# Kernel tuning notes

Hardware: AMD Instinct MI355X
Metric: run time of the kernel (lower is better)

## Reference

```python
import jax, jax.numpy as jnp
import numpy as np

BATCH, N_FEAT, N_CH = 16384, 16, 1
EXP_ORDER, OUT_DIM = 3, 256


def expansion_indices(n, exp_order):
    """Replicates the original nested-loop index bookkeeping statically.

    Returns a list of (J, P) per expansion pass: the new block of monomials is
    x[:, J, :] * epd[:, P, :]. All indices in a pass reference terms produced in
    earlier passes, so one concat per pass is exactly equivalent to the original.
    """
    Id = np.arange(n)
    M = n
    steps = []
    for _ in range(exp_order):
        Js, Ps = [], []
        for j in range(n):
            rng = np.arange(Id[j], Id[n - 1] + 1)
            Js.append(np.full(rng.shape, j))
            Ps.append(rng)
            Id[j] = M
            M += rng.size
        steps.append((np.concatenate(Js), np.concatenate(Ps)))
    return steps, M

STEPS, M_TOTAL = expansion_indices(N_FEAT, EXP_ORDER)  # M_TOTAL == 4844


def taylor_expand(x):
    # x: [B, n, Q] -> epd: [B, M_TOTAL, Q] (all monomials of degree 1..EXP_ORDER+1)
    epd = x
    for J, P in STEPS:
        new = x[:, J, :] * epd[:, P, :]
        epd = jnp.concatenate([epd, new], axis=1)
    return epd


def setup_inputs() -> dict:
    key = jax.random.key(0)
    k1, k2, k3 = jax.random.split(key, 3)
    inputs = jax.random.normal(k1, (BATCH, N_FEAT, N_CH), dtype=jnp.float32)
    # 'dl' weight init: uniform(-1/sqrt(shape[0]), 1/sqrt(shape[0]))
    w_scale = 1.0 / np.sqrt(OUT_DIM)
    W = jax.random.uniform(k2, (OUT_DIM, M_TOTAL), minval=-w_scale, maxval=w_scale, dtype=jnp.float32)
    # 'uniform' bias init: uniform(-0.2, 0.2), shape [out, 1]
    b = jax.random.uniform(k3, (OUT_DIM, 1), minval=-0.2, maxval=0.2, dtype=jnp.float32)
    return {"inputs": inputs, "W": W, "b": b}


def reference(inputs, W, b):
    # cp_type='tanh': first cp block applies tanh, second block is identity for tanh
    x = jnp.tanh(inputs)
    epd = taylor_expand(x)                         # [B, M_TOTAL, Q]
    out = jnp.einsum('rm,bmq->brq', W, epd) + b    # [B, OUT_DIM, Q]
    return jax.nn.relu(out)                        # act_type='relu'
```

## Files before the change

kernel.cpp:

```cpp
#include <hip/hip_runtime.h>

#define BATCH   16384
#define NF      16
#define OUTD    256
#define NNEW    4828
#define MTOT    4844
#define KPAD    4864
#define KPAD2   (KPAD/2)
#define NCHUNK  76
#define TROW    155
#define ASTR    72

struct ExpTab { unsigned jp[NNEW]; int total; };

constexpr ExpTab make_tab() {
    ExpTab t{};
    int Id[NF] = {};
    for (int i = 0; i < NF; ++i) Id[i] = i;
    int M = NF, idx = 0;
    for (int pass = 0; pass < 3; ++pass) {
        const int hi = Id[NF - 1];
        for (int j = 0; j < NF; ++j) {
            const int lo = Id[j];
            for (int p = lo; p <= hi; ++p) t.jp[idx++] = ((unsigned)j << 16) | (unsigned)p;
            Id[j] = M;
            M += hi - lo + 1;
        }
    }
    t.total = M;
    return t;
}
constexpr ExpTab h_tab = make_tab();
static_assert(h_tab.total == MTOT, "M_TOTAL");

struct PkTab {
    alignas(16) unsigned e[KPAD];
    unsigned b2[136];
};

constexpr PkTab make_pk() {
    ExpTab t = make_tab();
    int d2[NF][NF] = {};
    {
        int m = NF;
        for (int j = 0; j < NF; ++j)
            for (int p = j; p < NF; ++p) d2[j][p] = m++;
    }
    PkTab pk{};
    for (int q = 0; q < 136; ++q) {
        unsigned jp = t.jp[q];
        pk.b2[q] = (jp >> 16) | ((jp & 0xffffu) << 16);
    }
    for (int m = 0; m < KPAD; ++m) {
        if (m >= MTOT) { pk.e[m] = 153u | (153u << 16); continue; }
        int f[4] = {}, n = 0, cur = m;
        while (cur >= NF) {
            unsigned jp = t.jp[cur - NF];
            f[n++] = (int)(jp >> 16);
            cur = (int)(jp & 0xffffu);
        }
        f[n++] = cur;
        for (int i = 0; i < n; ++i)
            for (int k = i + 1; k < n; ++k)
                if (f[k] < f[i]) { int tmp = f[i]; f[i] = f[k]; f[k] = tmp; }
        unsigned L, R;
        if      (n == 1) { L = (unsigned)f[0];         R = 152u; }
        else if (n == 2) { L = (unsigned)d2[f[0]][f[1]]; R = 152u; }
        else if (n == 3) { L = (unsigned)d2[f[0]][f[1]]; R = (unsigned)f[2]; }
        else             { L = (unsigned)d2[f[0]][f[1]]; R = (unsigned)d2[f[2]][f[3]]; }
        pk.e[m] = L | (R << 16);
    }
    return pk;
}
constexpr bool pk_ok() {
    PkTab p = make_pk();
    for (int m = 0; m < KPAD; ++m)
        if ((p.e[m] & 0xffffu) > 153u || (p.e[m] >> 16) > 153u) return false;
    return p.e[16] == (16u | (152u << 16));
}
static_assert(pk_ok(), "2-factor decomposition");

__device__ const PkTab g_pk = make_pk();

typedef __attribute__((ext_vector_type(8))) short    bf16x8;
typedef __attribute__((ext_vector_type(4))) float    f32x4;
typedef __attribute__((ext_vector_type(4))) unsigned uint4v;

__device__ inline unsigned bfpack2(float lo, float hi) {
    unsigned ul = __float_as_uint(lo), uh = __float_as_uint(hi);
    ul = (ul + 0x7fffu + ((ul >> 16) & 1u)) >> 16;
    uh = (uh + 0x7fffu + ((uh >> 16) & 1u)) & 0xffff0000u;
    return ul | uh;
}

__global__ __launch_bounds__(256) void wconv_kernel(
    const float* __restrict__ W, unsigned* __restrict__ Wb)
{
    const int r = blockIdx.x;
    for (int i = threadIdx.x; i < KPAD2; i += 256) {
        const int c0 = 2 * i, c1 = 2 * i + 1;
        const float f0 = (c0 < MTOT) ? W[(size_t)r * MTOT + c0] : 0.f;
        const float f1 = (c1 < MTOT) ? W[(size_t)r * MTOT + c1] : 0.f;
        Wb[(size_t)r * KPAD2 + i] = bfpack2(f0, f1);
    }
}

__global__ __launch_bounds__(512, 2) void fused_kernel(
    const float* __restrict__ x,
    const unsigned short* __restrict__ Wb,
    const float* __restrict__ bias,
    float* __restrict__ C)
{
    __shared__ float T[64 * TROW];
    __shared__ alignas(16) unsigned short As[2][64][ASTR];
    const int t   = threadIdx.x;
    const int l   = t & 63;
    const int wid = t >> 6;
    const size_t m0 = (size_t)blockIdx.x * 64;

    uint4v eA[4], eB[4];
    auto loadPk = [&](int c, uint4v (&e4)[4]) {
        const uint4v* pe = (const uint4v*)(g_pk.e + c * 64 + wid * 16);
#pragma unroll
        for (int i = 0; i < 4; ++i) e4[i] = pe[i];
    };
    if (wid < 4) loadPk(0, eA);

#pragma unroll
    for (int i = 0; i < 2; ++i) {
        const int v = t * 2 + i;
        const int r = v >> 4, fq = v & 15;
        T[r * TROW + fq] = tanhf(x[(m0 + r) * NF + fq]);
    }
    if (t < 64) { T[t * TROW + 152] = 1.0f; T[t * TROW + 153] = 0.0f; }
    __syncthreads();

    {
        const int r = t >> 3, s = t & 7, base = r * TROW;
#pragma unroll
        for (int i = 0; i < 17; ++i) {
            const int q = s + 8 * i;
            const unsigned e = g_pk.b2[q];
            T[base + NF + q] = T[base + (e & 0xffffu)] * T[base + (e >> 16)];
        }
    }
    __syncthreads();

    const int pbase = l * TROW;
    auto expand = [&](int slot, const uint4v (&e4)[4]) {
        float v[16];
#pragma unroll
        for (int i = 0; i < 16; ++i) {
            const unsigned e = e4[i >> 2][i & 3];
            v[i] = T[pbase + (e & 0xffffu)] * T[pbase + (e >> 16)];
        }
        uint4v o0, o1;
        o0[0] = bfpack2(v[0],  v[1]);  o0[1] = bfpack2(v[2],  v[3]);
        o0[2] = bfpack2(v[4],  v[5]);  o0[3] = bfpack2(v[6],  v[7]);
        o1[0] = bfpack2(v[8],  v[9]);  o1[1] = bfpack2(v[10], v[11]);
        o1[2] = bfpack2(v[12], v[13]); o1[3] = bfpack2(v[14], v[15]);
        *(uint4v*)&As[slot][l][wid * 16]     = o0;
        *(uint4v*)&As[slot][l][wid * 16 + 8] = o1;
    };

    const int w  = wid - 4;
    const int lr = l & 15, lk = l >> 4;
    const unsigned short* wbase = Wb + (size_t)(w * 64 + lr) * KPAD + lk * 8;
    bf16x8 bA[4][2], bB[4][2];
    auto prefB = [&](int c, bf16x8 (&bf)[4][2]) {
#pragma unroll
        for (int ni = 0; ni < 4; ++ni)
#pragma unroll
            for (int ks = 0; ks < 2; ++ks)
                bf[ni][ks] = *(const bf16x8*)(wbase + (size_t)ni * 16 * KPAD
                                              + (size_t)c * 64 + ks * 32);
    };
    f32x4 acc[4][4];
#pragma unroll
    for (int i = 0; i < 4; ++i)
#pragma unroll
        for (int j = 0; j < 4; ++j) acc[i][j] = (f32x4){0.f, 0.f, 0.f, 0.f};

    auto domfma = [&](int slot, bf16x8 (&bf)[4][2]) {
#pragma unroll
        for (int ks = 0; ks < 2; ++ks) {
            bf16x8 af[4];
#pragma unroll
            for (int mi = 0; mi < 4; ++mi)
                af[mi] = *(const bf16x8*)&As[slot][mi * 16 + lr][ks * 32 + lk * 8];
#pragma unroll
            for (int mi = 0; mi < 4; ++mi)
#pragma unroll
                for (int ni = 0; ni < 4; ++ni)
                    acc[mi][ni] = __builtin_amdgcn_mfma_f32_16x16x32_bf16(
                        af[mi], bf[ni][ks], acc[mi][ni], 0, 0, 0);
        }
    };

    if (wid < 4) { expand(0, eA); loadPk(1, eB); }
    else         { prefB(0, bA); }
    __syncthreads();

    for (int it = 0; it < NCHUNK / 2; ++it) {
        const int c = 2 * it;
        if (wid < 4) {
            if (c + 2 < NCHUNK) loadPk(c + 2, eA);
            expand(1, eB);
        } else {
            prefB(c + 1, bB);
            domfma(0, bA);
        }
        __syncthreads();
        if (wid < 4) {
            if (c + 3 < NCHUNK) loadPk(c + 3, eB);
            if (c + 2 < NCHUNK) expand(0, eA);
        } else {
            if (c + 2 < NCHUNK) prefB(c + 2, bA);
            domfma(1, bB);
        }
        __syncthreads();
    }

    if (wid >= 4) {
#pragma unroll
        for (int ni = 0; ni < 4; ++ni) {
            const int col = w * 64 + ni * 16 + lr;
            const float bv = bias[col];
#pragma unroll
            for (int mi = 0; mi < 4; ++mi) {
                const size_t r0 = m0 + mi * 16 + lk * 4;
#pragma unroll
                for (int j = 0; j < 4; ++j)
                    C[(r0 + j) * OUTD + col] = fmaxf(acc[mi][ni][j] + bv, 0.f);
            }
        }
    }
}

extern "C" void kernel_launch(void* const* d_in, const int* in_sizes, int n_in,
                              void* d_out, int out_size, void* d_ws, size_t ws_size,
                              hipStream_t stream)
{
    const float* x    = (const float*)d_in[0];
    const float* W    = (const float*)d_in[1];
    const float* bias = (const float*)d_in[2];
    float* out        = (float*)d_out;

    unsigned* Wb = (unsigned*)d_ws;
    wconv_kernel<<<OUTD, 256, 0, stream>>>(W, Wb);
    fused_kernel<<<BATCH / 64, 512, 0, stream>>>(
        x, (const unsigned short*)Wb, bias, out);
}
```

Baseline: 148.9 us.

## Halve batch tile to 32 rows with 2 producer and 4 MFMA waves

Each block now handles 32 batch rows instead of 64. It uses 384 threads: 2 waves expand monomials into LDS and 4 waves run MFMAs, with launch bounds changed to allow 3 blocks per CU. The A tile in LDS gets an XOR swizzle on 16-byte groups to cut bank conflicts, and the MFMA section is wrapped in s_setprio. The aim is more blocks (512 instead of 256) and better occupancy and latency hiding. The cost is that every W tile is reloaded from global/L2 for only 32 rows, doubling weight traffic per output.

```diff
diff --git a/kernel.cpp b/kernel.cpp
--- a/kernel.cpp
+++ b/kernel.cpp
@@ -8,6 +8,7 @@
 #define KPAD    4864
 #define KPAD2   (KPAD/2)
 #define NCHUNK  76
+#define BM      32
 #define TROW    155
 #define ASTR    72
 
@@ -64,7 +65,7 @@
             for (int k = i + 1; k < n; ++k)
                 if (f[k] < f[i]) { int tmp = f[i]; f[i] = f[k]; f[k] = tmp; }
         unsigned L, R;
-        if      (n == 1) { L = (unsigned)f[0];         R = 152u; }
+        if      (n == 1) { L = (unsigned)f[0];           R = 152u; }
         else if (n == 2) { L = (unsigned)d2[f[0]][f[1]]; R = 152u; }
         else if (n == 3) { L = (unsigned)d2[f[0]][f[1]]; R = (unsigned)f[2]; }
         else             { L = (unsigned)d2[f[0]][f[1]]; R = (unsigned)d2[f[2]][f[3]]; }
@@ -105,37 +106,54 @@
     }
 }
 
-__global__ __launch_bounds__(512, 2) void fused_kernel(
+__global__ __launch_bounds__(384, 3) void fused_kernel(
     const float* __restrict__ x,
     const unsigned short* __restrict__ Wb,
     const float* __restrict__ bias,
     float* __restrict__ C)
 {
-    __shared__ float T[64 * TROW];
-    __shared__ alignas(16) unsigned short As[2][64][ASTR];
+    __shared__ float T[BM * TROW];
+    __shared__ alignas(16) unsigned short As[2][BM * ASTR];
     const int t   = threadIdx.x;
     const int l   = t & 63;
     const int wid = t >> 6;
-    const size_t m0 = (size_t)blockIdx.x * 64;
-
+    const size_t m0 = (size_t)blockIdx.x * BM;
+
+    const int pr = l & 31;
+    const int ph = l >> 5;
     uint4v eA[4], eB[4];
     auto loadPk = [&](int c, uint4v (&e4)[4]) {
-        const uint4v* pe = (const uint4v*)(g_pk.e + c * 64 + wid * 16);
+        const uint4v* pe = (const uint4v*)(g_pk.e + c * 64 + wid * 32 + ph * 16);
 #pragma unroll
         for (int i = 0; i < 4; ++i) e4[i] = pe[i];
     };
-    if (wid < 4) loadPk(0, eA);
-
-#pragma unroll
-    for (int i = 0; i < 2; ++i) {
-        const int v = t * 2 + i;
-        const int r = v >> 4, fq = v & 15;
-        T[r * TROW + fq] = tanhf(x[(m0 + r) * NF + fq]);
-    }
-    if (t < 64) { T[t * TROW + 152] = 1.0f; T[t * TROW + 153] = 0.0f; }
+    if (wid < 2) loadPk(0, eA);
+
+    const int w  = wid - 2;
+    const int lr = l & 15, lk = l >> 4;
+    const unsigned short* wbase = Wb + (size_t)(w * 64 + lr) * KPAD + lk * 8;
+    bf16x8 bA[4][2], bB[4][2];
+    auto prefB = [&](int c, bf16x8 (&bf)[4][2]) {
+#pragma unroll
+        for (int ni = 0; ni < 4; ++ni)
+#pragma unroll
+            for (int ks = 0; ks < 2; ++ks)
+                bf[ni][ks] = *(const bf16x8*)(wbase + (size_t)ni * 16 * KPAD
+                                              + (size_t)c * 64 + ks * 32);
+    };
+    if (wid >= 2) prefB(0, bA);
+
+    if (t < 256) {
+#pragma unroll
+        for (int i = 0; i < 2; ++i) {
+            const int v = t * 2 + i;
+            const int r = v >> 4, fq = v & 15;
+            T[r * TROW + fq] = tanhf(x[(m0 + r) * NF + fq]);
+        }
+        if (t < BM) { T[t * TROW + 152] = 1.0f; T[t * TROW + 153] = 0.0f; }
+    }
     __syncthreads();
-
-    {
+    if (t < 256) {
         const int r = t >> 3, s = t & 7, base = r * TROW;
 #pragma unroll
         for (int i = 0; i < 17; ++i) {
@@ -146,7 +164,11 @@
     }
     __syncthreads();
 
-    const int pbase = l * TROW;
+    const int pbase = pr * TROW;
+    const int g0   = wid * 4 + ph * 2;
+    const int gswz = (pr >> 3) & 3;
+    const int wo0  = pr * ASTR + ((g0    ) ^ gswz) * 8;
+    const int wo1  = pr * ASTR + ((g0 + 1) ^ gswz) * 8;
     auto expand = [&](int slot, const uint4v (&e4)[4]) {
         float v[16];
 #pragma unroll
@@ -159,51 +181,44 @@
         o0[2] = bfpack2(v[4],  v[5]);  o0[3] = bfpack2(v[6],  v[7]);
         o1[0] = bfpack2(v[8],  v[9]);  o1[1] = bfpack2(v[10], v[11]);
         o1[2] = bfpack2(v[12], v[13]); o1[3] = bfpack2(v[14], v[15]);
-        *(uint4v*)&As[slot][l][wid * 16]     = o0;
-        *(uint4v*)&As[slot][l][wid * 16 + 8] = o1;
-    };
-
-    const int w  = wid - 4;
-    const int lr = l & 15, lk = l >> 4;
-    const unsigned short* wbase = Wb + (size_t)(w * 64 + lr) * KPAD + lk * 8;
-    bf16x8 bA[4][2], bB[4][2];
-    auto prefB = [&](int c, bf16x8 (&bf)[4][2]) {
-#pragma unroll
-        for (int ni = 0; ni < 4; ++ni)
-#pragma unroll
-            for (int ks = 0; ks < 2; ++ks)
-                bf[ni][ks] = *(const bf16x8*)(wbase + (size_t)ni * 16 * KPAD
-                                              + (size_t)c * 64 + ks * 32);
-    };
-    f32x4 acc[4][4];
-#pragma unroll
-    for (int i = 0; i < 4; ++i)
+        *(uint4v*)&As[slot][wo0] = o0;
+        *(uint4v*)&As[slot][wo1] = o1;
+    };
+
+    f32x4 acc[2][4];
+#pragma unroll
+    for (int i = 0; i < 2; ++i)
 #pragma unroll
         for (int j = 0; j < 4; ++j) acc[i][j] = (f32x4){0.f, 0.f, 0.f, 0.f};
 
     auto domfma = [&](int slot, bf16x8 (&bf)[4][2]) {
-#pragma unroll
-        for (int ks = 0; ks < 2; ++ks) {
-            bf16x8 af[4];
-#pragma unroll
-            for (int mi = 0; mi < 4; ++mi)
-                af[mi] = *(const bf16x8*)&As[slot][mi * 16 + lr][ks * 32 + lk * 8];
-#pragma unroll
-            for (int mi = 0; mi < 4; ++mi)
+        bf16x8 af[2][2];
+#pragma unroll
+        for (int mi = 0; mi < 2; ++mi)
+#pragma unroll
+            for (int ks = 0; ks < 2; ++ks) {
+                const int row = mi * 16 + lr;
+                const int sg  = (ks * 4 + lk) ^ ((row >> 3) & 3);
+                af[mi][ks] = *(const bf16x8*)&As[slot][row * ASTR + sg * 8];
+            }
+        __builtin_amdgcn_s_setprio(1);
+#pragma unroll
+        for (int ks = 0; ks < 2; ++ks)
+#pragma unroll
+            for (int mi = 0; mi < 2; ++mi)
 #pragma unroll
                 for (int ni = 0; ni < 4; ++ni)
                     acc[mi][ni] = __builtin_amdgcn_mfma_f32_16x16x32_bf16(
-                        af[mi], bf[ni][ks], acc[mi][ni], 0, 0, 0);
-        }
-    };
-
-    if (wid < 4) { expand(0, eA); loadPk(1, eB); }
-    else         { prefB(0, bA); }
+                        af[mi][ks], bf[ni][ks], acc[mi][ni], 0, 0, 0);
+        __builtin_amdgcn_s_setprio(0);
+    };
+
+    if (wid < 2) { expand(0, eA); loadPk(1, eB); }
     __syncthreads();
 
     for (int it = 0; it < NCHUNK / 2; ++it) {
         const int c = 2 * it;
-        if (wid < 4) {
+        if (wid < 2) {
             if (c + 2 < NCHUNK) loadPk(c + 2, eA);
             expand(1, eB);
         } else {
@@ -211,7 +226,7 @@
             domfma(0, bA);
         }
         __syncthreads();
-        if (wid < 4) {
+        if (wid < 2) {
             if (c + 3 < NCHUNK) loadPk(c + 3, eB);
             if (c + 2 < NCHUNK) expand(0, eA);
         } else {
@@ -221,13 +236,13 @@
         __syncthreads();
     }
 
-    if (wid >= 4) {
+    if (wid >= 2) {
 #pragma unroll
         for (int ni = 0; ni < 4; ++ni) {
             const int col = w * 64 + ni * 16 + lr;
             const float bv = bias[col];
 #pragma unroll
-            for (int mi = 0; mi < 4; ++mi) {
+            for (int mi = 0; mi < 2; ++mi) {
                 const size_t r0 = m0 + mi * 16 + lk * 4;
 #pragma unroll
                 for (int j = 0; j < 4; ++j)
@@ -248,6 +263,6 @@
 
     unsigned* Wb = (unsigned*)d_ws;
     wconv_kernel<<<OUTD, 256, 0, stream>>>(W, Wb);
-    fused_kernel<<<BATCH / 64, 512, 0, stream>>>(
+    fused_kernel<<<BATCH / BM, 384, 0, stream>>>(
         x, (const unsigned short*)Wb, bias, out);
 }
```

Result: slower. 299.2 us (+101.0%).

## Reorder monomial columns so expansion uses contiguous 4-wide runs and batch syncs

Applied to the files above, without the earlier changes.

Builds a compile-time permutation of the monomial columns, padded to 5120, so each group of 4 columns shares one left factor and a contiguous run of right factors. This cuts lookup-table loads and LDS reads in the expansion. The weight conversion kernel gathers W through the same permutation. The A buffer grows to 8 slots in a blocked layout held in dynamic shared memory, so each barrier now covers 4 chunks instead of 1. This reduces synchronisation count but adds padded columns and more LDS per block, which may reduce occupancy.

```diff
diff --git a/kernel.cpp b/kernel.cpp
--- a/kernel.cpp
+++ b/kernel.cpp
@@ -3,84 +3,86 @@
 #define BATCH   16384
 #define NF      16
 #define OUTD    256
-#define NNEW    4828
 #define MTOT    4844
-#define KPAD    4864
-#define KPAD2   (KPAD/2)
-#define NCHUNK  76
+#define NK      5120
+#define NCHUNK  80
+#define NIV     20
 #define TROW    155
-#define ASTR    72
-
-struct ExpTab { unsigned jp[NNEW]; int total; };
-
-constexpr ExpTab make_tab() {
-    ExpTab t{};
-    int Id[NF] = {};
-    for (int i = 0; i < NF; ++i) Id[i] = i;
-    int M = NF, idx = 0;
-    for (int pass = 0; pass < 3; ++pass) {
-        const int hi = Id[NF - 1];
-        for (int j = 0; j < NF; ++j) {
-            const int lo = Id[j];
-            for (int p = lo; p <= hi; ++p) t.jp[idx++] = ((unsigned)j << 16) | (unsigned)p;
-            Id[j] = M;
-            M += hi - lo + 1;
-        }
-    }
-    t.total = M;
-    return t;
-}
-constexpr ExpTab h_tab = make_tab();
-static_assert(h_tab.total == MTOT, "M_TOTAL");
-
-struct PkTab {
-    alignas(16) unsigned e[KPAD];
-    unsigned b2[136];
+#define NCREAL  5080
+
+struct Plan {
+    unsigned cplan[NCHUNK * 16];
+    short    perm[NK];
+    unsigned d2t[136];
+    int ncols; int nreal; bool ok;
 };
 
-constexpr PkTab make_pk() {
-    ExpTab t = make_tab();
-    int d2[NF][NF] = {};
-    {
-        int m = NF;
-        for (int j = 0; j < NF; ++j)
-            for (int p = j; p < NF; ++p) d2[j][p] = m++;
-    }
-    PkTab pk{};
-    for (int q = 0; q < 136; ++q) {
-        unsigned jp = t.jp[q];
-        pk.b2[q] = (jp >> 16) | ((jp & 0xffffu) << 16);
-    }
-    for (int m = 0; m < KPAD; ++m) {
-        if (m >= MTOT) { pk.e[m] = 153u | (153u << 16); continue; }
-        int f[4] = {}, n = 0, cur = m;
-        while (cur >= NF) {
-            unsigned jp = t.jp[cur - NF];
-            f[n++] = (int)(jp >> 16);
-            cur = (int)(jp & 0xffffu);
-        }
-        f[n++] = cur;
-        for (int i = 0; i < n; ++i)
-            for (int k = i + 1; k < n; ++k)
-                if (f[k] < f[i]) { int tmp = f[i]; f[i] = f[k]; f[k] = tmp; }
-        unsigned L, R;
-        if      (n == 1) { L = (unsigned)f[0];         R = 152u; }
-        else if (n == 2) { L = (unsigned)d2[f[0]][f[1]]; R = 152u; }
-        else if (n == 3) { L = (unsigned)d2[f[0]][f[1]]; R = (unsigned)f[2]; }
-        else             { L = (unsigned)d2[f[0]][f[1]]; R = (unsigned)d2[f[2]][f[3]]; }
-        pk.e[m] = L | (R << 16);
-    }
-    return pk;
-}
-constexpr bool pk_ok() {
-    PkTab p = make_pk();
-    for (int m = 0; m < KPAD; ++m)
-        if ((p.e[m] & 0xffffu) > 153u || (p.e[m] >> 16) > 153u) return false;
-    return p.e[16] == (16u | (152u << 16));
-}
-static_assert(pk_ok(), "2-factor decomposition");
-
-__device__ const PkTab g_pk = make_pk();
+constexpr Plan make_plan() {
+    Plan P{};
+    int posx[17] = {};
+    for (int c = 0; c <= 16; ++c) posx[c] = 17 * c - c * (c - 1) / 2;
+    int S1t[16], Id2t[16], b3[16], b4[16];
+    for (int j = 0; j < 16; ++j) { S1t[j] = 16 * j - j * (j - 1) / 2; Id2t[j] = 16 + S1t[j]; }
+    { int s = 152; for (int j = 0; j < 16; ++j) { b3[j] = s; s += 152 - Id2t[j]; } }
+    { int s = 968; for (int j = 0; j < 16; ++j) { b4[j] = s; s += 968 - b3[j]; } }
+    { int idx = 0;
+      for (int c = 0; c < 16; ++c)
+        for (int d = c; d < 16; ++d)
+            P.d2t[idx++] = (unsigned)posx[c] | ((unsigned)posx[d] << 10)
+                         | ((unsigned)(posx[c] + 1 + (d - c)) << 20);
+    }
+    for (int q = 0; q < NCHUNK * 16; ++q) P.cplan[q] = 153u | (152u << 16);
+    for (int k = 0; k < NK; ++k) P.perm[k] = -1;
+
+    int k = 0;
+    for (int p = 0; p < 152; ++p) {
+        if ((k & 3) == 0) P.cplan[k >> 2] = 152u | ((unsigned)p << 16);
+        int c = 0; while (posx[c + 1] <= p) ++c;
+        int m;
+        if (p == posx[c]) m = c;
+        else { int d = c + (p - posx[c] - 1); m = 16 + S1t[c] + (d - c); }
+        P.perm[k++] = (short)m;
+    }
+    for (int b = 0; b < 16; ++b)
+      for (int a = 0; a <= b; ++a) {
+        const int L = posx[a] + 1 + (b - a);
+        const int st = posx[b], len = 152 - st, plen = (len + 3) & ~3;
+        for (int off = 0; off < plen; ++off) {
+            if ((k & 3) == 0) P.cplan[k >> 2] = (unsigned)L | ((unsigned)(st + off) << 16);
+            if (off < len) {
+                const int p = st + off;
+                int c = 0; while (posx[c + 1] <= p) ++c;
+                int m;
+                if (p == posx[c]) {
+                    m = b3[a] + (16 + S1t[b] + (c - b)) - Id2t[a];
+                } else {
+                    const int d = c + (p - posx[c] - 1);
+                    const int o3 = b3[b] + (16 + S1t[c] + (d - c)) - Id2t[b];
+                    m = b4[a] + o3 - b3[a];
+                }
+                P.perm[k] = (short)m;
+            }
+            ++k;
+        }
+      }
+    P.ncols = k;
+    unsigned bm[152] = {};
+    int cnt = 0; bool ok = (k == NCREAL);
+    for (int kk = 0; kk < NK; ++kk) {
+        const int m = P.perm[kk];
+        if (m >= 0) {
+            if (m >= MTOT || (bm[m >> 5] & (1u << (m & 31)))) { ok = false; break; }
+            bm[m >> 5] |= 1u << (m & 31); ++cnt;
+        }
+    }
+    if (cnt != MTOT) ok = false;
+    P.nreal = cnt; P.ok = ok;
+    return P;
+}
+constexpr Plan h_plan = make_plan();
+static_assert(h_plan.ncols == NCREAL, "padded col count");
+static_assert(h_plan.ok, "perm bijection onto [0,4844)");
+__device__ const Plan g_plan = make_plan();
 
 typedef __attribute__((ext_vector_type(8))) short    bf16x8;
 typedef __attribute__((ext_vector_type(4))) float    f32x4;
@@ -97,13 +99,18 @@
     const float* __restrict__ W, unsigned* __restrict__ Wb)
 {
     const int r = blockIdx.x;
-    for (int i = threadIdx.x; i < KPAD2; i += 256) {
-        const int c0 = 2 * i, c1 = 2 * i + 1;
-        const float f0 = (c0 < MTOT) ? W[(size_t)r * MTOT + c0] : 0.f;
-        const float f1 = (c1 < MTOT) ? W[(size_t)r * MTOT + c1] : 0.f;
-        Wb[(size_t)r * KPAD2 + i] = bfpack2(f0, f1);
-    }
-}
+    const float* Wr = W + (size_t)r * MTOT;
+    for (int i = threadIdx.x; i < NK / 2; i += 256) {
+        const int m0 = g_plan.perm[2 * i], m1 = g_plan.perm[2 * i + 1];
+        const float f0 = (m0 >= 0) ? Wr[m0] : 0.f;
+        const float f1 = (m1 >= 0) ? Wr[m1] : 0.f;
+        Wb[(size_t)r * (NK / 2) + i] = bfpack2(f0, f1);
+    }
+}
+
+#define T_BYTES   (64 * TROW * 4)
+#define AS_BYTES  (8 * 8 * 64 * 8 * 2)
+#define LDS_BYTES (T_BYTES + AS_BYTES)
 
 __global__ __launch_bounds__(512, 2) void fused_kernel(
     const float* __restrict__ x,
@@ -111,113 +118,125 @@
     const float* __restrict__ bias,
     float* __restrict__ C)
 {
-    __shared__ float T[64 * TROW];
-    __shared__ alignas(16) unsigned short As[2][64][ASTR];
-    const int t   = threadIdx.x;
-    const int l   = t & 63;
-    const int wid = t >> 6;
+    extern __shared__ char smem[];
+    float* T = (float*)smem;
+    unsigned short* As = (unsigned short*)(smem + T_BYTES);
+
+    const int t = threadIdx.x, l = t & 63, wid = t >> 6;
     const size_t m0 = (size_t)blockIdx.x * 64;
 
-    uint4v eA[4], eB[4];
-    auto loadPk = [&](int c, uint4v (&e4)[4]) {
-        const uint4v* pe = (const uint4v*)(g_pk.e + c * 64 + wid * 16);
-#pragma unroll
-        for (int i = 0; i < 4; ++i) e4[i] = pe[i];
-    };
-    if (wid < 4) loadPk(0, eA);
+    uint4v ePA[4], ePB[4];
+    auto loadPlan = [&](int iv, uint4v (&e)[4]) {
+#pragma unroll
+        for (int cc = 0; cc < 4; ++cc)
+            e[cc] = *(const uint4v*)(g_plan.cplan + (iv * 4 + cc) * 16 + wid * 4);
+    };
+    const int w = wid - 4, lr = l & 15, lk = l >> 4;
+    const unsigned short* wbase = Wb + (size_t)(w * 64 + lr) * NK + lk * 8;
+    bf16x8 bA[4][2], bB[4][2];
+    auto prefB = [&](int c, bf16x8 (&bf)[4][2]) {
+#pragma unroll
+        for (int ni = 0; ni < 4; ++ni)
+#pragma unroll
+            for (int ks = 0; ks < 2; ++ks)
+                bf[ni][ks] = *(const bf16x8*)(wbase + (size_t)ni * 16 * NK
+                                              + (size_t)c * 64 + ks * 32);
+    };
+    if (wid < 4) loadPlan(0, ePA); else prefB(0, bA);
 
 #pragma unroll
     for (int i = 0; i < 2; ++i) {
         const int v = t * 2 + i;
-        const int r = v >> 4, fq = v & 15;
-        T[r * TROW + fq] = tanhf(x[(m0 + r) * NF + fq]);
-    }
-    if (t < 64) { T[t * TROW + 152] = 1.0f; T[t * TROW + 153] = 0.0f; }
+        const int r = v >> 4, f = v & 15;
+        const int pf = 17 * f - f * (f - 1) / 2;
+        T[r * TROW + pf] = tanhf(x[(m0 + r) * NF + f]);
+    }
+    if (t < 64) { T[t*TROW + 152] = 1.f; T[t*TROW + 153] = 0.f; T[t*TROW + 154] = 0.f; }
     __syncthreads();
-
     {
         const int r = t >> 3, s = t & 7, base = r * TROW;
 #pragma unroll
         for (int i = 0; i < 17; ++i) {
-            const int q = s + 8 * i;
-            const unsigned e = g_pk.b2[q];
-            T[base + NF + q] = T[base + (e & 0xffffu)] * T[base + (e >> 16)];
+            const unsigned e = g_plan.d2t[s + 8 * i];
+            T[base + (e >> 20)] = T[base + (e & 1023u)] * T[base + ((e >> 10) & 1023u)];
         }
     }
     __syncthreads();
 
-    const int pbase = l * TROW;
-    auto expand = [&](int slot, const uint4v (&e4)[4]) {
+    const int pb = l * TROW;
+    auto expand = [&](int c, const uint4v& e) {
         float v[16];
 #pragma unroll
-        for (int i = 0; i < 16; ++i) {
-            const unsigned e = e4[i >> 2][i & 3];
-            v[i] = T[pbase + (e & 0xffffu)] * T[pbase + (e >> 16)];
+        for (int q = 0; q < 4; ++q) {
+            const unsigned eq = e[q];
+            const float lv = T[pb + (eq & 0xffffu)];
+            const int   r0 = pb + (int)(eq >> 16);
+#pragma unroll
+            for (int u = 0; u < 4; ++u) v[q * 4 + u] = lv * T[r0 + u];
         }
         uint4v o0, o1;
-        o0[0] = bfpack2(v[0],  v[1]);  o0[1] = bfpack2(v[2],  v[3]);
-        o0[2] = bfpack2(v[4],  v[5]);  o0[3] = bfpack2(v[6],  v[7]);
-        o1[0] = bfpack2(v[8],  v[9]);  o1[1] = bfpack2(v[10], v[11]);
-        o1[2] = bfpack2(v[12], v[13]); o1[3] = bfpack2(v[14], v[15]);
-        *(uint4v*)&As[slot][l][wid * 16]     = o0;
-        *(uint4v*)&As[slot][l][wid * 16 + 8] = o1;
-    };
-
-    const int w  = wid - 4;
-    const int lr = l & 15, lk = l >> 4;
-    const unsigned short* wbase = Wb + (size_t)(w * 64 + lr) * KPAD + lk * 8;
-    bf16x8 bA[4][2], bB[4][2];
-    auto prefB = [&](int c, bf16x8 (&bf)[4][2]) {
-#pragma unroll
-        for (int ni = 0; ni < 4; ++ni)
+        o0[0]=bfpack2(v[0],v[1]);   o0[1]=bfpack2(v[2],v[3]);
+        o0[2]=bfpack2(v[4],v[5]);   o0[3]=bfpack2(v[6],v[7]);
+        o1[0]=bfpack2(v[8],v[9]);   o1[1]=bfpack2(v[10],v[11]);
+        o1[2]=bfpack2(v[12],v[13]); o1[3]=bfpack2(v[14],v[15]);
+        const int slot = c & 7;
+        *(uint4v*)&As[(((slot * 8 + 2 * wid    ) * 64) + l) * 8] = o0;
+        *(uint4v*)&As[(((slot * 8 + 2 * wid + 1) * 64) + l) * 8] = o1;
+    };
+
+    f32x4 acc[4][4];
+#pragma unroll
+    for (int i = 0; i < 4; ++i)
+#pragma unroll
+        for (int j = 0; j < 4; ++j) acc[i][j] = (f32x4){0.f, 0.f, 0.f, 0.f};
+
+    auto domfma = [&](int c, bf16x8 (&bf)[4][2]) {
+        const int slot = c & 7;
+        bf16x8 af[4][2];
+#pragma unroll
+        for (int mi = 0; mi < 4; ++mi)
 #pragma unroll
             for (int ks = 0; ks < 2; ++ks)
-                bf[ni][ks] = *(const bf16x8*)(wbase + (size_t)ni * 16 * KPAD
-                                              + (size_t)c * 64 + ks * 32);
-    };
-    f32x4 acc[4][4];
-#pragma unroll
-    for (int i = 0; i < 4; ++i)
-#pragma unroll
-        for (int j = 0; j < 4; ++j) acc[i][j] = (f32x4){0.f, 0.f, 0.f, 0.f};
-
-    auto domfma = [&](int slot, bf16x8 (&bf)[4][2]) {
-#pragma unroll
-        for (int ks = 0; ks < 2; ++ks) {
-            bf16x8 af[4];
-#pragma unroll
-            for (int mi = 0; mi < 4; ++mi)
-                af[mi] = *(const bf16x8*)&As[slot][mi * 16 + lr][ks * 32 + lk * 8];
+                af[mi][ks] = *(const bf16x8*)
+                    &As[(((slot * 8 + ks * 4 + lk) * 64) + mi * 16 + lr) * 8];
+#pragma unroll
+        for (int ks = 0; ks < 2; ++ks)
 #pragma unroll
             for (int mi = 0; mi < 4; ++mi)
 #pragma unroll
                 for (int ni = 0; ni < 4; ++ni)
                     acc[mi][ni] = __builtin_amdgcn_mfma_f32_16x16x32_bf16(
-                        af[mi], bf[ni][ks], acc[mi][ni], 0, 0, 0);
-        }
-    };
-
-    if (wid < 4) { expand(0, eA); loadPk(1, eB); }
-    else         { prefB(0, bA); }
+                        af[mi][ks], bf[ni][ks], acc[mi][ni], 0, 0, 0);
+    };
+
+    auto pbody = [&](int i, uint4v (&eUse)[4], uint4v (&eLoad)[4]) {
+        if (i + 1 < NIV) {
+#pragma unroll
+            for (int cc = 0; cc < 4; ++cc) expand((i + 1) * 4 + cc, eUse[cc]);
+        }
+        if (i + 2 < NIV) loadPlan(i + 2, eLoad);
+    };
+    auto cbody = [&](int i) {
+#pragma unroll
+        for (int cc = 0; cc < 4; ++cc) {
+            const int c = i * 4 + cc;
+            const int nc = (c + 1 < NCHUNK) ? c + 1 : c;
+            if (cc & 1) { prefB(nc, bA); domfma(c, bB); }
+            else        { prefB(nc, bB); domfma(c, bA); }
+        }
+    };
+
+    if (wid < 4) {
+#pragma unroll
+        for (int cc = 0; cc < 4; ++cc) expand(cc, ePA[cc]);
+        loadPlan(1, ePB);
+    }
     __syncthreads();
 
-    for (int it = 0; it < NCHUNK / 2; ++it) {
-        const int c = 2 * it;
-        if (wid < 4) {
-            if (c + 2 < NCHUNK) loadPk(c + 2, eA);
-            expand(1, eB);
-        } else {
-            prefB(c + 1, bB);
-            domfma(0, bA);
-        }
+    for (int i2 = 0; i2 < NIV; i2 += 2) {
+        if (wid < 4) pbody(i2, ePB, ePA); else cbody(i2);
         __syncthreads();
-        if (wid < 4) {
-            if (c + 3 < NCHUNK) loadPk(c + 3, eB);
-            if (c + 2 < NCHUNK) expand(0, eA);
-        } else {
-            if (c + 2 < NCHUNK) prefB(c + 2, bA);
-            domfma(1, bB);
-        }
+        if (wid < 4) pbody(i2 + 1, ePA, ePB); else cbody(i2 + 1);
         __syncthreads();
     }
 
@@ -247,7 +266,9 @@
     float* out        = (float*)d_out;
 
     unsigned* Wb = (unsigned*)d_ws;
+    (void)hipFuncSetAttribute((const void*)fused_kernel,
+                              hipFuncAttributeMaxDynamicSharedMemorySize, LDS_BYTES);
     wconv_kernel<<<OUTD, 256, 0, stream>>>(W, Wb);
-    fused_kernel<<<BATCH / 64, 512, 0, stream>>>(
+    fused_kernel<<<BATCH / 64, 512, LDS_BYTES, stream>>>(
         x, (const unsigned short*)Wb, bias, out);
 }
```

After: 151.7 us. Within noise of the previous version (+1.9%).
